# Kernel optimization log

Hardware: AMD Instinct MI355X
Metric: run time of the kernel (lower is better)

## Reference

```python
import jax, jax.numpy as jnp
import numpy as np

B, N = 32, 512
N_DIM, N_P, N_K = 128, 3, 2
F0_DIM = N_DIM * N_P            # 384
CAT_DIM = N_DIM * (N_K + 1) * N_P  # 1152


def setup_inputs() -> dict:
    key = jax.random.key(0)
    ks = jax.random.split(key, 12)
    s = 0.05
    return {
        "loc": jax.random.uniform(ks[0], (B, N, 2), dtype=jnp.float32),
        "deadline": jax.random.uniform(ks[1], (B, N), dtype=jnp.float32),
        "workload": jax.random.uniform(ks[2], (B, N), dtype=jnp.float32),
        "depot": jax.random.uniform(ks[3], (B, 1, 2), dtype=jnp.float32),
        "W_init": jax.random.normal(ks[4], (3, F0_DIM), dtype=jnp.float32) * s,
        "b_init": jnp.zeros((F0_DIM,), jnp.float32),
        "W_dep": jax.random.normal(ks[5], (2, N_DIM), dtype=jnp.float32) * s,
        "b_dep": jnp.zeros((N_DIM,), jnp.float32),
        "W_g1": jax.random.normal(ks[6], (CAT_DIM, N_DIM), dtype=jnp.float32) * s,
        "b_g1": jnp.zeros((N_DIM,), jnp.float32),
        "W_g2": jax.random.normal(ks[7], (CAT_DIM, N_DIM), dtype=jnp.float32) * s,
        "b_g2": jnp.zeros((N_DIM,), jnp.float32),
        "W_g3": jax.random.normal(ks[8], (CAT_DIM, N_DIM), dtype=jnp.float32) * s,
        "b_g3": jnp.zeros((N_DIM,), jnp.float32),
        "gamma": jnp.ones((F0_DIM,), jnp.float32),
        "beta": jnp.zeros((F0_DIM,), jnp.float32),
        "W_F": jax.random.normal(ks[9], (F0_DIM, N_DIM), dtype=jnp.float32) * s,
        "b_F": jnp.zeros((N_DIM,), jnp.float32),
    }


def _forward(loc, deadline, workload, depot, W_init, b_init, W_dep, b_dep,
             W_g1, b_g1, W_g2, b_g2, W_g3, b_g3, gamma, beta, W_F, b_F):
    # X = [loc, deadline/deadline.max()] -> [B,N,3] (workload is concatenated then dropped in original)
    X = jnp.concatenate([loc, (deadline / deadline.max())[..., None]], axis=-1)
    n = X.shape[1]
    # pairwise squared distances [B,N,N]
    d2 = ((X[:, :, None, :] - X[:, None, :, :]) ** 2).sum(-1)
    off = ~jnp.eye(n, dtype=bool)                      # off-diagonal mask
    d2_safe = jnp.where(off, d2, 1.0)
    A = jnp.where(off, 1.0 / jnp.sqrt(d2_safe), 0.0)   # A = 1/dist off-diag, 0 on diag
    A = jnp.where(jnp.isnan(A), 0.0, A)                # A[A!=A]=0
    A = A / A.max()                                    # global max-normalize
    deg = A.sum(-1) - 1.0                              # (A.sum(-1) - 1)
    L = jnp.eye(n, dtype=A.dtype) * deg[:, None, :] - A  # D - A (diag = deg)
    L2 = L @ L

    F0 = X @ W_init + b_init                           # [B,N,384]
    F0_sq = F0 * F0
    F0_cu = F0 * F0_sq

    def prop(F):
        return jnp.concatenate([F, L @ F, L2 @ F], axis=-1)  # [B,N,1152]

    g1 = prop(F0) @ W_g1 + b_g1
    g2 = prop(F0_sq) @ W_g2 + b_g2
    g3 = prop(F0_cu) @ W_g3 + b_g3
    F1 = jnp.concatenate([g1, g2, g3], axis=-1)        # [B,N,384]
    F1 = jax.nn.leaky_relu(F1) + F0

    # BatchNorm1d (training mode): stats over flattened (B*N) samples, biased var
    flat = F1.reshape(-1, F1.shape[-1])
    mu = flat.mean(0)
    var = ((flat - mu) ** 2).mean(0)
    F1 = (F1 - mu) / jnp.sqrt(var + 1e-5) * gamma + beta

    F_final = jax.nn.leaky_relu(F1 @ W_F + b_F)        # [B,N,128]
    dep = depot @ W_dep + b_dep                        # [B,1,128]
    h = jnp.concatenate([dep, F_final], axis=1)        # [B,N+1,128]
    return h, h.mean(axis=1)


def reference(loc, deadline, workload, depot, W_init, b_init, W_dep, b_dep,
              W_g1, b_g1, W_g2, b_g2, W_g3, b_g3, gamma, beta, W_F, b_F):
    return _forward(loc, deadline, workload, depot, W_init, b_init, W_dep, b_dep,
                    W_g1, b_g1, W_g2, b_g2, W_g3, b_g3, gamma, beta, W_F, b_F)
```

## Files before the change

kernel.cpp:

```cpp
#include <hip/hip_runtime.h>

#define LEAKY(x) ((x) > 0.0f ? (x) : 0.01f * (x))

typedef __attribute__((ext_vector_type(8))) short bf16x8;
typedef __attribute__((ext_vector_type(4))) float f32x4;
typedef __attribute__((ext_vector_type(8))) unsigned short u16x8;
typedef __attribute__((ext_vector_type(4))) unsigned short u16x4;

__device__ __forceinline__ unsigned short f2bf(float f) {
    unsigned int u = __float_as_uint(f);
    unsigned int r = (u + 0x7fffu + ((u >> 16) & 1u)) >> 16;
    return (unsigned short)r;
}
__device__ __forceinline__ float bf2f(unsigned short u) {
    return __uint_as_float(((unsigned int)u) << 16);
}

#define GLD16(gp, lp) __builtin_amdgcn_global_load_lds( \
    (__attribute__((address_space(1))) void*)(gp), \
    (__attribute__((address_space(3))) void*)(lp), 16, 0, 0)


__global__ void k_dmax(const float* __restrict__ deadline, float* __restrict__ dmax) {
    int t = threadIdx.x;
    float m = deadline[blockIdx.x * 256 + t];
    for (int off = 32; off > 0; off >>= 1) m = fmaxf(m, __shfl_down(m, off));
    __shared__ float s[4];
    if ((t & 63) == 0) s[t >> 6] = m;
    __syncthreads();
    if (t == 0) atomicMax((unsigned int*)dmax,
                          __float_as_uint(fmaxf(fmaxf(s[0], s[1]), fmaxf(s[2], s[3]))));
}

__global__ __launch_bounds__(256) void k_rowstats(const float* __restrict__ loc,
                                                  const float* __restrict__ deadline,
                                                  const float* __restrict__ dmaxv,
                                                  float* __restrict__ rowsum, float* __restrict__ pmax64) {
    int blk = blockIdx.x;
    int wave = threadIdx.x >> 6, lane = threadIdx.x & 63;
    int bi = blk * 4 + wave;
    int b = bi >> 9, i = bi & 511;
    float invd = 1.0f / (*dmaxv);
    const float* lb = loc + b * 1024;
    const float* db = deadline + b * 512;
    float xi = lb[i * 2], yi = lb[i * 2 + 1], zi = db[i] * invd;
    float lsum = 0.f, lmax = 0.f;
    for (int j = lane; j < 512; j += 64) {
        float d0 = xi - lb[j * 2], d1 = yi - lb[j * 2 + 1], d2 = zi - db[j] * invd;
        float dd = d0 * d0 + d1 * d1 + d2 * d2;
        float r = (j == i) ? 0.f : rsqrtf(dd);
        lsum += r; lmax = fmaxf(lmax, r);
    }
    for (int off = 32; off > 0; off >>= 1) {
        lsum += __shfl_down(lsum, off);
        lmax = fmaxf(lmax, __shfl_down(lmax, off));
    }
    __shared__ float smax[4];
    if (lane == 0) { rowsum[bi] = lsum; smax[wave] = lmax; }
    __syncthreads();
    if (threadIdx.x == 0) {
        float m = fmaxf(fmaxf(smax[0], smax[1]), fmaxf(smax[2], smax[3]));
        atomicMax((unsigned int*)(pmax64 + (blk & 63)), __float_as_uint(m));
    }
}

__global__ __launch_bounds__(256) void k_build(
    const float* __restrict__ loc, const float* __restrict__ deadline,
    const float* __restrict__ dmaxv, const float* __restrict__ rowsum,
    const float* __restrict__ pmax64,
    const float* __restrict__ Wi, const float* __restrict__ bi_,
    const float* __restrict__ Wg1, const float* __restrict__ Wg2, const float* __restrict__ Wg3,
    unsigned short* __restrict__ Lb,
    unsigned short* __restrict__ P1, unsigned short* __restrict__ P2, unsigned short* __restrict__ P3,
    unsigned short* __restrict__ WgT)
{
    __shared__ float amaxS;
    int blk = blockIdx.x;
    int t = threadIdx.x;
    if (blk < 8192) {
        if (t < 64) {
            float m = pmax64[t];
            for (int off = 32; off > 0; off >>= 1) m = fmaxf(m, __shfl_down(m, off));
            if (t == 0) amaxS = m;
        }
        __syncthreads();
        float inv = 1.0f / amaxS;
        float invd = 1.0f / (*dmaxv);
        int id = blk * 256 + t;
        size_t e = (size_t)id * 4;
        size_t bi = e >> 9;
        int b = (int)(bi >> 9);
        int i = (int)(bi & 511);
        int j0 = (int)(e & 511);
        const float* lb = loc + b * 1024;
        const float* db = deadline + b * 512;
        float xi = lb[i * 2], yi = lb[i * 2 + 1], zi = db[i] * invd;
        float4 l01 = *(const float4*)(lb + j0 * 2);
        float4 l23 = *(const float4*)(lb + j0 * 2 + 4);
        float4 dj = *(const float4*)(db + j0);
        float diag = rowsum[bi] * inv - 1.0f;
        float jx[4] = {l01.x, l01.z, l23.x, l23.z};
        float jy[4] = {l01.y, l01.w, l23.y, l23.w};
        float jz[4] = {dj.x * invd, dj.y * invd, dj.z * invd, dj.w * invd};
        u16x4 o;
#pragma unroll
        for (int j = 0; j < 4; j++) {
            float d0 = xi - jx[j], d1 = yi - jy[j], d2 = zi - jz[j];
            float dd = d0 * d0 + d1 * d1 + d2 * d2;
            float v = (i == j0 + j) ? diag : -rsqrtf(dd) * inv;
            o[j] = f2bf(v);
        }
        *(u16x4*)(Lb + e) = o;
    } else if (blk < 14336) {
        int id = (blk - 8192) * 256 + t;
        int row = id / 96, c4 = (id % 96) * 4;
        float x0 = loc[row * 2], x1 = loc[row * 2 + 1], x2 = deadline[row] / (*dmaxv);
        float4 w0 = *(const float4*)(Wi + c4);
        float4 w1 = *(const float4*)(Wi + 384 + c4);
        float4 w2 = *(const float4*)(Wi + 768 + c4);
        float4 bb = *(const float4*)(bi_ + c4);
        float f[4] = {x0 * w0.x + x1 * w1.x + x2 * w2.x + bb.x,
                      x0 * w0.y + x1 * w1.y + x2 * w2.y + bb.y,
                      x0 * w0.z + x1 * w1.z + x2 * w2.z + bb.z,
                      x0 * w0.w + x1 * w1.w + x2 * w2.w + bb.w};
        u16x4 o1, o2, o3;
#pragma unroll
        for (int j = 0; j < 4; j++) {
            o1[j] = f2bf(f[j]); o2[j] = f2bf(f[j] * f[j]); o3[j] = f2bf(f[j] * f[j] * f[j]);
        }
        size_t e = (size_t)row * 384 + c4;
        *(u16x4*)(P1 + e) = o1; *(u16x4*)(P2 + e) = o2; *(u16x4*)(P3 + e) = o3;
    } else {
        int id = (blk - 14336) * 256 + t;
        int part = id / 147456, rem = id % 147456;
        int g = rem / 384, k = rem % 384;
        int kp = g >> 7, n = g & 127;
        const float* W = (kp == 0) ? Wg1 : (kp == 1 ? Wg2 : Wg3);
        WgT[id] = f2bf(W[(part * 384 + k) * 128 + n]);
    }
}


__device__ __forceinline__ void pipe128x128(
    const unsigned short* __restrict__ A0, int As0, const unsigned short* __restrict__ B0, int Bs0, int it0,
    const unsigned short* __restrict__ A1, int As1, const unsigned short* __restrict__ B1, int Bs1, int it1,
    unsigned short* AsL, unsigned short* BsL,
    f32x4 (&acc)[4][4], int t)
{
    const int lane = t & 63, wave = t >> 6;
    const int wm = wave >> 1, wn = wave & 1;
    const int quad = lane >> 4, l16 = lane & 15;
    const int lrow = lane >> 3;
    const int lsw  = ((lane & 7) ^ lrow) * 8;
    const int total = it0 + it1;

    auto stage = [&](int buf, int s) {
        int sg = (s >= it0);
        const unsigned short* A = sg ? A1 : A0;
        const unsigned short* B = sg ? B1 : B0;
        int As = sg ? As1 : As0, Bs = sg ? Bs1 : Bs0;
        int k0 = (sg ? (s - it0) : s) * 64;
#pragma unroll
        for (int j = 0; j < 4; j++) {
            int r0 = wave * 32 + j * 8;
            GLD16(A + (size_t)(r0 + lrow) * As + k0 + lsw, AsL + buf * 8192 + r0 * 64);
            GLD16(B + (size_t)(r0 + lrow) * Bs + k0 + lsw, BsL + buf * 8192 + r0 * 64);
        }
    };

    stage(0, 0);
    if (total > 1) stage(1, 1);
    for (int s = 0; s < total; s++) {
        const int buf = s & 1;
        if (s + 1 < total) asm volatile("s_waitcnt vmcnt(8)" ::: "memory");
        else               asm volatile("s_waitcnt vmcnt(0)" ::: "memory");
        __builtin_amdgcn_s_barrier();
        __builtin_amdgcn_sched_barrier(0);
        bf16x8 af[2][4], bfr[2][4];
#pragma unroll
        for (int h = 0; h < 2; h++) {
            int phys = ((h * 4 + quad) ^ (l16 & 7)) * 8;
#pragma unroll
            for (int i = 0; i < 4; i++)
                af[h][i] = *(const bf16x8*)(AsL + buf * 8192 + (wm * 64 + i * 16 + l16) * 64 + phys);
#pragma unroll
            for (int n = 0; n < 4; n++)
                bfr[h][n] = *(const bf16x8*)(BsL + buf * 8192 + (wn * 64 + n * 16 + l16) * 64 + phys);
        }
        asm volatile("s_waitcnt lgkmcnt(0)" ::: "memory");
        __builtin_amdgcn_sched_barrier(0);
        __builtin_amdgcn_s_barrier();
        __builtin_amdgcn_sched_barrier(0);
        if (s + 2 < total) stage(buf, s + 2);
#pragma unroll
        for (int h = 0; h < 2; h++)
#pragma unroll
            for (int i = 0; i < 4; i++)
#pragma unroll
                for (int n = 0; n < 4; n++)
                    acc[i][n] = __builtin_amdgcn_mfma_f32_16x16x32_bf16(af[h][i], bfr[h][n], acc[i][n], 0, 0, 0);
    }
}

__device__ __forceinline__ void pipe64x64(
    const unsigned short* __restrict__ A0, int As0, const unsigned short* __restrict__ B0, int Bs0, int it0,
    unsigned short* AsL, unsigned short* BsL,
    f32x4 (&acc)[2][2], int t)
{
    const int lane = t & 63, wave = t >> 6;
    const int wm = wave >> 1, wn = wave & 1;
    const int quad = lane >> 4, l16 = lane & 15;
    const int lrow = lane >> 3;
    const int lsw  = ((lane & 7) ^ lrow) * 8;

    auto stage = [&](int buf, int s) {
        int k0 = s * 64;
#pragma unroll
        for (int j = 0; j < 2; j++) {
            int r0 = wave * 16 + j * 8;
            GLD16(A0 + (size_t)(r0 + lrow) * As0 + k0 + lsw, AsL + buf * 4096 + r0 * 64);
            GLD16(B0 + (size_t)(r0 + lrow) * Bs0 + k0 + lsw, BsL + buf * 4096 + r0 * 64);
        }
    };

    stage(0, 0);
    if (it0 > 1) stage(1, 1);
    for (int s = 0; s < it0; s++) {
        const int buf = s & 1;
        if (s + 1 < it0) asm volatile("s_waitcnt vmcnt(4)" ::: "memory");
        else             asm volatile("s_waitcnt vmcnt(0)" ::: "memory");
        __builtin_amdgcn_s_barrier();
        __builtin_amdgcn_sched_barrier(0);
        bf16x8 af[2][2], bfr[2][2];
#pragma unroll
        for (int h = 0; h < 2; h++) {
            int phys = ((h * 4 + quad) ^ (l16 & 7)) * 8;
#pragma unroll
            for (int i = 0; i < 2; i++)
                af[h][i] = *(const bf16x8*)(AsL + buf * 4096 + (wm * 32 + i * 16 + l16) * 64 + phys);
#pragma unroll
            for (int n = 0; n < 2; n++)
                bfr[h][n] = *(const bf16x8*)(BsL + buf * 4096 + (wn * 32 + n * 16 + l16) * 64 + phys);
        }
        asm volatile("s_waitcnt lgkmcnt(0)" ::: "memory");
        __builtin_amdgcn_sched_barrier(0);
        __builtin_amdgcn_s_barrier();
        __builtin_amdgcn_sched_barrier(0);
        if (s + 2 < it0) stage(buf, s + 2);
#pragma unroll
        for (int h = 0; h < 2; h++)
#pragma unroll
            for (int i = 0; i < 2; i++)
#pragma unroll
                for (int n = 0; n < 2; n++)
                    acc[i][n] = __builtin_amdgcn_mfma_f32_16x16x32_bf16(af[h][i], bfr[h][n], acc[i][n], 0, 0, 0);
    }
}

__global__ __launch_bounds__(256) void k_ygemmT(
    const unsigned short* __restrict__ WgT,
    const unsigned short* __restrict__ P1, const unsigned short* __restrict__ P2,
    const unsigned short* __restrict__ P3, unsigned short* __restrict__ Y2T)
{
    __shared__ unsigned short AsL[16384], BsL[16384];
    const int t = threadIdx.x;
    const int id = blockIdx.x;
    const int b = id & 31, tt = id >> 5;
    const int kp = tt >> 2, nb = tt & 3;
    const unsigned short* P = (kp == 0) ? P1 : (kp == 1 ? P2 : P3);
    f32x4 acc[4][4];
#pragma unroll
    for (int i = 0; i < 4; i++)
#pragma unroll
        for (int n = 0; n < 4; n++) acc[i][n] = (f32x4){0.f, 0.f, 0.f, 0.f};
    pipe128x128(WgT + ((size_t)2 * 384 + kp * 128) * 384, 384,
                P + ((size_t)b * 512 + nb * 128) * 384, 384, 6,
                nullptr, 0, nullptr, 0, 0, AsL, BsL, acc, t);

    const int wave = t >> 6, lane = t & 63;
    const int wm = wave >> 1, wn = wave & 1;
    const int quad = lane >> 4, l16 = lane & 15;
#pragma unroll
    for (int i = 0; i < 4; i++)
#pragma unroll
        for (int n = 0; n < 4; n++) {
            int g = kp * 128 + wm * 64 + i * 16 + quad * 4;
            int node = nb * 128 + wn * 64 + n * 16 + l16;
#pragma unroll
            for (int r = 0; r < 4; r++)
                Y2T[((size_t)b * 384 + g + r) * 512 + node] = f2bf(acc[i][n][r]);
        }
}

__global__ __launch_bounds__(256) void k_lg1T(
    const unsigned short* __restrict__ Lb, const unsigned short* __restrict__ Y2T,
    const unsigned short* __restrict__ WgT,
    const unsigned short* __restrict__ P1, const unsigned short* __restrict__ P2,
    const unsigned short* __restrict__ P3, unsigned short* __restrict__ ZT)
{
    __shared__ unsigned short AsL[16384], BsL[16384];
    const int t = threadIdx.x;
    const int id = blockIdx.x;
    const int b = id & 31, tt = id >> 5;
    const int kp = tt >> 2, nb = tt & 3;
    const unsigned short* P = (kp == 0) ? P1 : (kp == 1 ? P2 : P3);
    f32x4 acc[4][4];
#pragma unroll
    for (int i = 0; i < 4; i++)
#pragma unroll
        for (int n = 0; n < 4; n++) acc[i][n] = (f32x4){0.f, 0.f, 0.f, 0.f};
    pipe128x128(Y2T + (size_t)b * 196608 + (size_t)kp * 128 * 512, 512,
                Lb + (size_t)b * 262144 + (size_t)nb * 128 * 512, 512, 8,
                WgT + ((size_t)1 * 384 + kp * 128) * 384, 384,
                P + ((size_t)b * 512 + nb * 128) * 384, 384, 6, AsL, BsL, acc, t);

    const int wave = t >> 6, lane = t & 63;
    const int wm = wave >> 1, wn = wave & 1;
    const int quad = lane >> 4, l16 = lane & 15;
#pragma unroll
    for (int i = 0; i < 4; i++)
#pragma unroll
        for (int n = 0; n < 4; n++) {
            int g = kp * 128 + wm * 64 + i * 16 + quad * 4;
            int node = nb * 128 + wn * 64 + n * 16 + l16;
#pragma unroll
            for (int r = 0; r < 4; r++)
                ZT[((size_t)b * 384 + g + r) * 512 + node] = f2bf(acc[i][n][r]);
        }
}

__global__ __launch_bounds__(256) void k_lg2(
    const unsigned short* __restrict__ Lb, const unsigned short* __restrict__ ZT,
    const unsigned short* __restrict__ WgT,
    const unsigned short* __restrict__ P1, const unsigned short* __restrict__ P2,
    const unsigned short* __restrict__ P3,
    const float* __restrict__ bg1, const float* __restrict__ bg2, const float* __restrict__ bg3,
    unsigned short* __restrict__ F1b, float* __restrict__ bn1, float* __restrict__ bn2)
{
    __shared__ unsigned short AsL[16384], BsL[16384];
    __shared__ float bnS[128], bnQ[128];
    const int t = threadIdx.x;
    const int id = blockIdx.x;
    const int b = id & 31, tt = id >> 5;
    const int mb = tt & 3, gt = tt >> 2;
    if (t < 128) { bnS[t] = 0.f; bnQ[t] = 0.f; }
    const unsigned short* P = (gt == 0) ? P1 : (gt == 1 ? P2 : P3);
    f32x4 acc[4][4];
#pragma unroll
    for (int i = 0; i < 4; i++)
#pragma unroll
        for (int n = 0; n < 4; n++) acc[i][n] = (f32x4){0.f, 0.f, 0.f, 0.f};
    pipe128x128(Lb + (size_t)b * 262144 + (size_t)mb * 128 * 512, 512,
                ZT + (size_t)b * 196608 + (size_t)gt * 128 * 512, 512, 8,
                P + ((size_t)b * 512 + mb * 128) * 384, 384,
                WgT + (size_t)(gt * 128) * 384, 384, 6,
                AsL, BsL, acc, t);

    const int wave = t >> 6, lane = t & 63;
    const int wm = wave >> 1, wn = wave & 1;
    const int quad = lane >> 4, l16 = lane & 15;
    const float* bg = (gt == 0) ? bg1 : (gt == 1 ? bg2 : bg3);
    float ls1[4], ls2[4];
#pragma unroll
    for (int n = 0; n < 4; n++) { ls1[n] = 0.f; ls2[n] = 0.f; }
#pragma unroll
    for (int i = 0; i < 4; i++) {
        int rowl = mb * 128 + wm * 64 + i * 16 + quad * 4;
        size_t rowg = (size_t)b * 512 + rowl;
#pragma unroll
        for (int n = 0; n < 4; n++) {
            int nloc = wn * 64 + n * 16 + l16;
            int g = gt * 128 + nloc;
            float bias = bg[nloc];
#pragma unroll
            for (int r = 0; r < 4; r++) {
                size_t idx = (rowg + r) * 384 + g;
                float c = acc[i][n][r] + bias;
                float v = LEAKY(c) + bf2f(P1[idx]);
                F1b[idx] = f2bf(v);
                ls1[n] += v; ls2[n] += v * v;
            }
        }
    }
#pragma unroll
    for (int n = 0; n < 4; n++) {
        int nloc = wn * 64 + n * 16 + l16;
        atomicAdd(&bnS[nloc], ls1[n]);
        atomicAdd(&bnQ[nloc], ls2[n]);
    }
    __syncthreads();
    if (t < 128) {
        atomicAdd(&bn1[gt * 128 + t], bnS[t]);
        atomicAdd(&bn2[gt * 128 + t], bnQ[t]);
    }
}

__global__ __launch_bounds__(256) void k_bnfold(
    const float* __restrict__ bn1, const float* __restrict__ bn2,
    const float* __restrict__ gamma, const float* __restrict__ beta,
    const float* __restrict__ WF, const float* __restrict__ bF,
    unsigned short* __restrict__ WFsT, float* __restrict__ beffv)
{
    int blk = blockIdx.x;
    if (blk < 192) {
        int id = blk * 256 + threadIdx.x;
        int n = id / 384, k = id % 384;
        float mu = bn1[k] * (1.f / 16384.f);
        float var = bn2[k] * (1.f / 16384.f) - mu * mu;
        float sc = gamma[k] / sqrtf(var + 1e-5f);
        WFsT[id] = f2bf(WF[k * 128 + n] * sc);
    } else {
        __shared__ float ttL[384];
        int c = threadIdx.x;
        for (int k = c; k < 384; k += 256) {
            float mu = bn1[k] * (1.f / 16384.f);
            float var = bn2[k] * (1.f / 16384.f) - mu * mu;
            float sc = gamma[k] / sqrtf(var + 1e-5f);
            ttL[k] = beta[k] - mu * sc;
        }
        __syncthreads();
        if (c < 128) {
            float a = bF[c];
            for (int k = 0; k < 384; k++) a += ttL[k] * WF[k * 128 + c];
            beffv[c] = a;
        }
    }
}

__global__ __launch_bounds__(256) void k_fgemm(
    const unsigned short* __restrict__ F1b, const unsigned short* __restrict__ WFsT,
    const float* __restrict__ beffv, float* __restrict__ out, float* __restrict__ msum)
{
    __shared__ unsigned short AsL[8192], BsL[8192];
    __shared__ float msS[64];
    const int t = threadIdx.x;
    const int id = blockIdx.x;
    const int b = id & 31, tt = id >> 5;
    const int seg = tt >> 1, nt = tt & 1;
    if (t < 64) msS[t] = 0.f;
    f32x4 acc[2][2];
#pragma unroll
    for (int i = 0; i < 2; i++)
#pragma unroll
        for (int n = 0; n < 2; n++) acc[i][n] = (f32x4){0.f, 0.f, 0.f, 0.f};
    pipe64x64(F1b + ((size_t)b * 512 + seg * 64) * 384, 384,
              WFsT + (size_t)nt * 64 * 384, 384, 6, AsL, BsL, acc, t);

    const int wave = t >> 6, lane = t & 63;
    const int wm = wave >> 1, wn = wave & 1;
    const int quad = lane >> 4, l16 = lane & 15;
    float ls[2];
#pragma unroll
    for (int n = 0; n < 2; n++) ls[n] = 0.f;
#pragma unroll
    for (int i = 0; i < 2; i++) {
        int nd = seg * 64 + wm * 32 + i * 16 + quad * 4;
#pragma unroll
        for (int n = 0; n < 2; n++) {
            int col = nt * 64 + wn * 32 + n * 16 + l16;
            float bb = beffv[col];
#pragma unroll
            for (int r = 0; r < 4; r++) {
                float x = acc[i][n][r] + bb;
                float v = LEAKY(x);
                out[(size_t)b * 65664 + (size_t)(nd + r + 1) * 128 + col] = v;
                ls[n] += v;
            }
        }
    }
#pragma unroll
    for (int n = 0; n < 2; n++) atomicAdd(&msS[wn * 32 + n * 16 + l16], ls[n]);
    __syncthreads();
    if (t < 64) atomicAdd(&msum[b * 128 + nt * 64 + t], msS[t]);
}

__global__ void k_meandep(const float* __restrict__ depot, const float* __restrict__ Wd,
                          const float* __restrict__ bd, const float* __restrict__ msum,
                          float* __restrict__ out) {
    int id = blockIdx.x * 256 + threadIdx.x;
    int b = id >> 7, o = id & 127;
    float dep = depot[b * 2] * Wd[o] + depot[b * 2 + 1] * Wd[128 + o] + bd[o];
    out[(size_t)b * 65664 + o] = dep;
    out[2101248 + id] = (msum[id] + dep) * (1.0f / 513.0f);
}


extern "C" void kernel_launch(void* const* d_in, const int* in_sizes, int n_in,
                              void* d_out, int out_size, void* d_ws, size_t ws_size,
                              hipStream_t stream) {
    const float* loc      = (const float*)d_in[0];
    const float* deadline = (const float*)d_in[1];
    const float* depot    = (const float*)d_in[3];
    const float* W_init   = (const float*)d_in[4];
    const float* b_init   = (const float*)d_in[5];
    const float* W_dep    = (const float*)d_in[6];
    const float* b_dep    = (const float*)d_in[7];
    const float* W_g1     = (const float*)d_in[8];
    const float* b_g1     = (const float*)d_in[9];
    const float* W_g2     = (const float*)d_in[10];
    const float* b_g2     = (const float*)d_in[11];
    const float* W_g3     = (const float*)d_in[12];
    const float* b_g3     = (const float*)d_in[13];
    const float* gamma    = (const float*)d_in[14];
    const float* beta     = (const float*)d_in[15];
    const float* W_F      = (const float*)d_in[16];
    const float* b_F      = (const float*)d_in[17];
    float* out = (float*)d_out;
    float* ws  = (float*)d_ws;

    float* dmaxv  = ws + 0;
    float* pmax64 = ws + 4;
    float* bn1    = ws + 68;
    float* bn2    = ws + 452;
    float* msum   = ws + 836;
    float* rowsum = ws + 4932;
    float* beffv  = ws + 21316;
    unsigned short* Lb   = (unsigned short*)(ws + 21448);
    unsigned short* P1   = (unsigned short*)(ws + 4215752);
    unsigned short* P2   = (unsigned short*)(ws + 7361480);
    unsigned short* P3   = (unsigned short*)(ws + 10507208);
    unsigned short* WgT  = (unsigned short*)(ws + 13652936);
    unsigned short* WFsT = (unsigned short*)(ws + 13874120);
    unsigned short* Y2T  = (unsigned short*)(ws + 13898696);
    unsigned short* ZT   = (unsigned short*)(ws + 17044424);
    unsigned short* F1b  = (unsigned short*)(ws + 20190152);

    hipMemsetAsync(ws, 0, 4932 * sizeof(float), stream);

    k_dmax<<<64, 256, 0, stream>>>(deadline, dmaxv);
    k_rowstats<<<4096, 256, 0, stream>>>(loc, deadline, dmaxv, rowsum, pmax64);
    k_build<<<16064, 256, 0, stream>>>(loc, deadline, dmaxv, rowsum, pmax64,
                                       W_init, b_init, W_g1, W_g2, W_g3,
                                       Lb, P1, P2, P3, WgT);

    k_ygemmT<<<384, 256, 0, stream>>>(WgT, P1, P2, P3, Y2T);
    k_lg1T<<<384, 256, 0, stream>>>(Lb, Y2T, WgT, P1, P2, P3, ZT);
    k_lg2<<<384, 256, 0, stream>>>(Lb, ZT, WgT, P1, P2, P3,
                                   b_g1, b_g2, b_g3, F1b, bn1, bn2);

    k_bnfold<<<193, 256, 0, stream>>>(bn1, bn2, gamma, beta, W_F, b_F, WFsT, beffv);
    k_fgemm<<<512, 256, 0, stream>>>(F1b, WFsT, beffv, out, msum);
    k_meandep<<<16, 256, 0, stream>>>(depot, W_dep, b_dep, msum, out);
}
```

Measured before the change: 222.6 us.

## Fuse BN fold, final GEMM and depot/mean epilogue into one kernel

Result: slower. 240.5 us (+8.0%).

```diff
diff --git a/kernel.cpp b/kernel.cpp
--- a/kernel.cpp
+++ b/kernel.cpp
@@ -202,61 +202,6 @@
     }
 }
 
-__device__ __forceinline__ void pipe64x64(
-    const unsigned short* __restrict__ A0, int As0, const unsigned short* __restrict__ B0, int Bs0, int it0,
-    unsigned short* AsL, unsigned short* BsL,
-    f32x4 (&acc)[2][2], int t)
-{
-    const int lane = t & 63, wave = t >> 6;
-    const int wm = wave >> 1, wn = wave & 1;
-    const int quad = lane >> 4, l16 = lane & 15;
-    const int lrow = lane >> 3;
-    const int lsw  = ((lane & 7) ^ lrow) * 8;
-
-    auto stage = [&](int buf, int s) {
-        int k0 = s * 64;
-#pragma unroll
-        for (int j = 0; j < 2; j++) {
-            int r0 = wave * 16 + j * 8;
-            GLD16(A0 + (size_t)(r0 + lrow) * As0 + k0 + lsw, AsL + buf * 4096 + r0 * 64);
-            GLD16(B0 + (size_t)(r0 + lrow) * Bs0 + k0 + lsw, BsL + buf * 4096 + r0 * 64);
-        }
-    };
-
-    stage(0, 0);
-    if (it0 > 1) stage(1, 1);
-    for (int s = 0; s < it0; s++) {
-        const int buf = s & 1;
-        if (s + 1 < it0) asm volatile("s_waitcnt vmcnt(4)" ::: "memory");
-        else             asm volatile("s_waitcnt vmcnt(0)" ::: "memory");
-        __builtin_amdgcn_s_barrier();
-        __builtin_amdgcn_sched_barrier(0);
-        bf16x8 af[2][2], bfr[2][2];
-#pragma unroll
-        for (int h = 0; h < 2; h++) {
-            int phys = ((h * 4 + quad) ^ (l16 & 7)) * 8;
-#pragma unroll
-            for (int i = 0; i < 2; i++)
-                af[h][i] = *(const bf16x8*)(AsL + buf * 4096 + (wm * 32 + i * 16 + l16) * 64 + phys);
-#pragma unroll
-            for (int n = 0; n < 2; n++)
-                bfr[h][n] = *(const bf16x8*)(BsL + buf * 4096 + (wn * 32 + n * 16 + l16) * 64 + phys);
-        }
-        asm volatile("s_waitcnt lgkmcnt(0)" ::: "memory");
-        __builtin_amdgcn_sched_barrier(0);
-        __builtin_amdgcn_s_barrier();
-        __builtin_amdgcn_sched_barrier(0);
-        if (s + 2 < it0) stage(buf, s + 2);
-#pragma unroll
-        for (int h = 0; h < 2; h++)
-#pragma unroll
-            for (int i = 0; i < 2; i++)
-#pragma unroll
-                for (int n = 0; n < 2; n++)
-                    acc[i][n] = __builtin_amdgcn_mfma_f32_16x16x32_bf16(af[h][i], bfr[h][n], acc[i][n], 0, 0, 0);
-    }
-}
-
 __global__ __launch_bounds__(256) void k_ygemmT(
     const unsigned short* __restrict__ WgT,
     const unsigned short* __restrict__ P1, const unsigned short* __restrict__ P2,
@@ -395,60 +340,110 @@
     }
 }
 
-__global__ __launch_bounds__(256) void k_bnfold(
+__global__ __launch_bounds__(256) void k_fgemm2(
+    const unsigned short* __restrict__ F1b,
     const float* __restrict__ bn1, const float* __restrict__ bn2,
     const float* __restrict__ gamma, const float* __restrict__ beta,
     const float* __restrict__ WF, const float* __restrict__ bF,
-    unsigned short* __restrict__ WFsT, float* __restrict__ beffv)
+    const float* __restrict__ depot, const float* __restrict__ Wd, const float* __restrict__ bd,
+    float* __restrict__ out, float* __restrict__ msum, unsigned int* __restrict__ donecnt)
 {
-    int blk = blockIdx.x;
-    if (blk < 192) {
-        int id = blk * 256 + threadIdx.x;
-        int n = id / 384, k = id % 384;
-        float mu = bn1[k] * (1.f / 16384.f);
-        float var = bn2[k] * (1.f / 16384.f) - mu * mu;
-        float sc = gamma[k] / sqrtf(var + 1e-5f);
-        WFsT[id] = f2bf(WF[k * 128 + n] * sc);
-    } else {
-        __shared__ float ttL[384];
-        int c = threadIdx.x;
-        for (int k = c; k < 384; k += 256) {
-            float mu = bn1[k] * (1.f / 16384.f);
-            float var = bn2[k] * (1.f / 16384.f) - mu * mu;
-            float sc = gamma[k] / sqrtf(var + 1e-5f);
-            ttL[k] = beta[k] - mu * sc;
-        }
-        __syncthreads();
-        if (c < 128) {
-            float a = bF[c];
-            for (int k = 0; k < 384; k++) a += ttL[k] * WF[k * 128 + c];
-            beffv[c] = a;
-        }
-    }
-}
-
-__global__ __launch_bounds__(256) void k_fgemm(
-    const unsigned short* __restrict__ F1b, const unsigned short* __restrict__ WFsT,
-    const float* __restrict__ beffv, float* __restrict__ out, float* __restrict__ msum)
-{
-    __shared__ unsigned short AsL[8192], BsL[8192];
-    __shared__ float msS[64];
+    __shared__ unsigned short Bs[24576];
+    __shared__ unsigned short As[8192];
+    __shared__ float scS[384], ttS[384];
+    __shared__ float beffS[64], beffF[64], msS[64];
+    __shared__ unsigned int lastFlag;
+
     const int t = threadIdx.x;
     const int id = blockIdx.x;
     const int b = id & 31, tt = id >> 5;
     const int seg = tt >> 1, nt = tt & 1;
-    if (t < 64) msS[t] = 0.f;
-    f32x4 acc[2][2];
-#pragma unroll
-    for (int i = 0; i < 2; i++)
-#pragma unroll
-        for (int n = 0; n < 2; n++) acc[i][n] = (f32x4){0.f, 0.f, 0.f, 0.f};
-    pipe64x64(F1b + ((size_t)b * 512 + seg * 64) * 384, 384,
-              WFsT + (size_t)nt * 64 * 384, 384, 6, AsL, BsL, acc, t);
-
-    const int wave = t >> 6, lane = t & 63;
+
+    for (int k = t; k < 384; k += 256) {
+        float mu = bn1[k] * (1.f / 16384.f);
+        float var = bn2[k] * (1.f / 16384.f) - mu * mu;
+        float sc = gamma[k] / sqrtf(var + 1e-5f);
+        scS[k] = sc;
+        ttS[k] = beta[k] - mu * sc;
+    }
+    if (t < 64) { beffS[t] = 0.f; msS[t] = 0.f; }
+    __syncthreads();
+
+    {
+        const int row = t & 63;
+        const int wfc = nt * 64 + row;
+        const int kg = t >> 6;
+        float bacc = 0.f;
+#pragma unroll 4
+        for (int j = 0; j < 12; j++) {
+            int c = kg * 12 + j;
+            int k0 = c * 8;
+            u16x8 pk;
+#pragma unroll
+            for (int e = 0; e < 8; e++) {
+                float w = WF[(size_t)(k0 + e) * 128 + wfc];
+                pk[e] = f2bf(w * scS[k0 + e]);
+                bacc += ttS[k0 + e] * w;
+            }
+            *(u16x8*)(Bs + (c >> 3) * 4096 + row * 64 + ((c & 7) ^ (row & 7)) * 8) = pk;
+        }
+        atomicAdd(&beffS[row], bacc);
+    }
+    __syncthreads();
+    if (t < 64) beffF[t] = bF[nt * 64 + t] + beffS[t];
+
+    const int lane = t & 63, wave = t >> 6;
     const int wm = wave >> 1, wn = wave & 1;
     const int quad = lane >> 4, l16 = lane & 15;
+    const int lrow = lane >> 3;
+    const int lsw  = ((lane & 7) ^ lrow) * 8;
+    const unsigned short* A0 = F1b + ((size_t)b * 512 + seg * 64) * 384;
+    f32x4 acc[2][2];
+#pragma unroll
+    for (int i = 0; i < 2; i++)
+#pragma unroll
+        for (int n = 0; n < 2; n++) acc[i][n] = (f32x4){0.f, 0.f, 0.f, 0.f};
+
+    auto stageA = [&](int buf, int s) {
+        int k0 = s * 64;
+#pragma unroll
+        for (int j = 0; j < 2; j++) {
+            int r0 = wave * 16 + j * 8;
+            GLD16(A0 + (size_t)(r0 + lrow) * 384 + k0 + lsw, As + buf * 4096 + r0 * 64);
+        }
+    };
+    stageA(0, 0); stageA(1, 1);
+    for (int s = 0; s < 6; s++) {
+        const int buf = s & 1;
+        if (s + 1 < 6) asm volatile("s_waitcnt vmcnt(2)" ::: "memory");
+        else           asm volatile("s_waitcnt vmcnt(0)" ::: "memory");
+        __builtin_amdgcn_s_barrier();
+        __builtin_amdgcn_sched_barrier(0);
+        bf16x8 af[2][2], bfr[2][2];
+#pragma unroll
+        for (int h = 0; h < 2; h++) {
+            int phys = ((h * 4 + quad) ^ (l16 & 7)) * 8;
+#pragma unroll
+            for (int i = 0; i < 2; i++)
+                af[h][i] = *(const bf16x8*)(As + buf * 4096 + (wm * 32 + i * 16 + l16) * 64 + phys);
+#pragma unroll
+            for (int n = 0; n < 2; n++)
+                bfr[h][n] = *(const bf16x8*)(Bs + s * 4096 + (wn * 32 + n * 16 + l16) * 64 + phys);
+        }
+        asm volatile("s_waitcnt lgkmcnt(0)" ::: "memory");
+        __builtin_amdgcn_sched_barrier(0);
+        __builtin_amdgcn_s_barrier();
+        __builtin_amdgcn_sched_barrier(0);
+        if (s + 2 < 6) stageA(buf, s + 2);
+#pragma unroll
+        for (int h = 0; h < 2; h++)
+#pragma unroll
+            for (int i = 0; i < 2; i++)
+#pragma unroll
+                for (int n = 0; n < 2; n++)
+                    acc[i][n] = __builtin_amdgcn_mfma_f32_16x16x32_bf16(af[h][i], bfr[h][n], acc[i][n], 0, 0, 0);
+    }
+
     float ls[2];
 #pragma unroll
     for (int n = 0; n < 2; n++) ls[n] = 0.f;
@@ -457,8 +452,9 @@
         int nd = seg * 64 + wm * 32 + i * 16 + quad * 4;
 #pragma unroll
         for (int n = 0; n < 2; n++) {
-            int col = nt * 64 + wn * 32 + n * 16 + l16;
-            float bb = beffv[col];
+            int lcol = wn * 32 + n * 16 + l16;
+            int col = nt * 64 + lcol;
+            float bb = beffF[lcol];
 #pragma unroll
             for (int r = 0; r < 4; r++) {
                 float x = acc[i][n][r] + bb;
@@ -472,16 +468,23 @@
     for (int n = 0; n < 2; n++) atomicAdd(&msS[wn * 32 + n * 16 + l16], ls[n]);
     __syncthreads();
     if (t < 64) atomicAdd(&msum[b * 128 + nt * 64 + t], msS[t]);
-}
-
-__global__ void k_meandep(const float* __restrict__ depot, const float* __restrict__ Wd,
-                          const float* __restrict__ bd, const float* __restrict__ msum,
-                          float* __restrict__ out) {
-    int id = blockIdx.x * 256 + threadIdx.x;
-    int b = id >> 7, o = id & 127;
-    float dep = depot[b * 2] * Wd[o] + depot[b * 2 + 1] * Wd[128 + o] + bd[o];
-    out[(size_t)b * 65664 + o] = dep;
-    out[2101248 + id] = (msum[id] + dep) * (1.0f / 513.0f);
+    __syncthreads();
+
+    if (t == 0) {
+        __threadfence();
+        unsigned int old = atomicAdd(donecnt, 1u);
+        lastFlag = (old == 511u) ? 1u : 0u;
+    }
+    __syncthreads();
+    if (lastFlag) {
+        for (int i = t; i < 4096; i += 256) {
+            int bb = i >> 7, o = i & 127;
+            float dep = depot[bb * 2] * Wd[o] + depot[bb * 2 + 1] * Wd[128 + o] + bd[o];
+            out[(size_t)bb * 65664 + o] = dep;
+            float ms = atomicAdd(&msum[i], 0.f);
+            out[2101248 + i] = (ms + dep) * (1.0f / 513.0f);
+        }
+    }
 }
 
 
@@ -509,18 +512,17 @@
     float* ws  = (float*)d_ws;
 
     float* dmaxv  = ws + 0;
+    unsigned int* donecnt = (unsigned int*)(ws + 2);
     float* pmax64 = ws + 4;
     float* bn1    = ws + 68;
     float* bn2    = ws + 452;
     float* msum   = ws + 836;
     float* rowsum = ws + 4932;
-    float* beffv  = ws + 21316;
     unsigned short* Lb   = (unsigned short*)(ws + 21448);
     unsigned short* P1   = (unsigned short*)(ws + 4215752);
     unsigned short* P2   = (unsigned short*)(ws + 7361480);
     unsigned short* P3   = (unsigned short*)(ws + 10507208);
     unsigned short* WgT  = (unsigned short*)(ws + 13652936);
-    unsigned short* WFsT = (unsigned short*)(ws + 13874120);
     unsigned short* Y2T  = (unsigned short*)(ws + 13898696);
     unsigned short* ZT   = (unsigned short*)(ws + 17044424);
     unsigned short* F1b  = (unsigned short*)(ws + 20190152);
@@ -538,7 +540,6 @@
     k_lg2<<<384, 256, 0, stream>>>(Lb, ZT, WgT, P1, P2, P3,
                                    b_g1, b_g2, b_g3, F1b, bn1, bn2);
 
-    k_bnfold<<<193, 256, 0, stream>>>(bn1, bn2, gamma, beta, W_F, b_F, WFsT, beffv);
-    k_fgemm<<<512, 256, 0, stream>>>(F1b, WFsT, beffv, out, msum);
-    k_meandep<<<16, 256, 0, stream>>>(depot, W_dep, b_dep, msum, out);
-}
+    k_fgemm2<<<512, 256, 0, stream>>>(F1b, bn1, bn2, gamma, beta, W_F, b_F,
+                                      depot, W_dep, b_dep, out, msum, donecnt);
+}
```
